# Kernel tuning notes

Measured on AMD Instinct MI355X. Metric: run time of the kernel, lower is better.

The kernel has to match this reference:

```python
import jax, jax.numpy as jnp
import numpy as np

B, C, D, Q = 256, 1000, 128, 262144
PROTO_M = 0.99   # args.proto_m
TEMP = 0.01      # hardcoded temperature in forward


def setup_inputs() -> dict:
    key = jax.random.key(0)
    ks = jax.random.split(key, 8)
    return {
        'q': jax.random.normal(ks[0], (B, D), jnp.float32),
        'k': jax.random.normal(ks[1], (B, D), jnp.float32),
        'output': jax.random.normal(ks[2], (B, C), jnp.float32),
        'output2': jax.random.normal(ks[3], (B, C), jnp.float32),
        'partial_Y': (jax.random.uniform(ks[4], (B, C)) < 0.1).astype(jnp.float32),
        'prototypes': jax.random.normal(ks[5], (C, D), jnp.float32),
        'queue': jax.random.normal(ks[6], (Q, D), jnp.float32),
        'queue_pseudo': jax.random.uniform(ks[7], (Q,), dtype=jnp.float32),
    }


def reference(q, k, output, output2, partial_Y, prototypes, queue, queue_pseudo):
    # pseudo-label selection: softmax over (detached logits * candidate mask) / T
    predicted_scores = jax.nn.softmax(jax.lax.stop_gradient(output) * partial_Y / TEMP, axis=1)
    pseudo_labels_b = jnp.argmax(predicted_scores, axis=1)  # [B] int

    # prototype scores use prototypes BEFORE the EMA update (mm snapshots values)
    logits_prot = jnp.matmul(jax.lax.stop_gradient(q), prototypes.T)  # [B, C]
    score_prot = jax.nn.softmax(logits_prot, axis=1)

    # sequential per-sample EMA scatter into prototypes (order-dependent on dup labels)
    q_detached = jax.lax.stop_gradient(q)

    def ema_step(protos, xs):
        feat, lab = xs
        new_row = protos[lab] * PROTO_M + (1.0 - PROTO_M) * feat
        return protos.at[lab].set(new_row), None

    protos, _ = jax.lax.scan(ema_step, prototypes, (q_detached, pseudo_labels_b))
    # F.normalize(p=2, dim=1) with eps=1e-12 clamp
    protos = protos / jnp.maximum(jnp.linalg.norm(protos, axis=1, keepdims=True), 1e-12)

    features = jnp.concatenate([q, k, queue], axis=0)  # [2B+Q, D]
    pseudo_labels = jnp.concatenate([
        pseudo_labels_b.astype(jnp.float32),
        pseudo_labels_b.astype(jnp.float32),
        queue_pseudo,
    ], axis=0)  # [2B+Q]

    return (output, output2, features, pseudo_labels, score_prot, protos)
```

## Files before the change

### kernel.cpp

```cpp
#include <hip/hip_runtime.h>
#include <math.h>

#define B 256
#define C 1000
#define D 128
#define QN 262144

#define OFF_FEAT   512000
#define OFF_LBL    34131968
#define OFF_SCORE  34394624
#define OFF_PROTO  34650624

#define N_Q4   (QN * D / 4)
#define N_O4   (B * C / 4)
#define N_F4   (B * D / 4)
#define N_P4   (QN / 4)

#define DST_Q4   ((OFF_FEAT + 2 * B * D) / 4)
#define DST_O24  (B * C / 4)
#define DST_QF4  (OFF_FEAT / 4)
#define DST_KF4  (OFF_FEAT / 4 + N_F4)
#define DST_P4   ((OFF_LBL + 2 * B) / 4)

#define SM_O2  (N_O4)
#define SM_Q   (2 * N_O4)
#define SM_K   (2 * N_O4 + N_F4)
#define SM_P   (2 * N_O4 + 2 * N_F4)
#define SM_TOT (2 * N_O4 + 2 * N_F4 + N_P4)

#define Q_TILES   (N_Q4 / 1024)
#define K1_TILES  640
#define POOL_BASE4 ((size_t)K1_TILES * 1024)
#define POOL_N4    ((size_t)(Q_TILES - K1_TILES) * 1024)

#define R1_SP     256
#define R1_SM     512
#define SM_BLKS   ((SM_TOT + 255) / 256)
#define R1_CP     (R1_SM + SM_BLKS)
#define K1_GRID   (R1_CP + K1_TILES)

#define K3_GRID   4096

__global__ __launch_bounds__(256) void k1_kernel(
    const float* __restrict__ q,
    const float* __restrict__ kk,
    const float* __restrict__ output,
    const float* __restrict__ output2,
    const float* __restrict__ partial_Y,
    const float* __restrict__ prototypes,
    const float4* __restrict__ queue,
    const float* __restrict__ queue_pseudo,
    int* __restrict__ labels,
    float* __restrict__ out)
{
    const int bid = blockIdx.x;
    const int tid = threadIdx.x;
    __shared__ float smem[1384];

    if (bid < B) {
        float* sv = smem;
        int*   si = (int*)(smem + 256);
        const float* row = output + (size_t)bid * C;
        const float* msk = partial_Y + (size_t)bid * C;

        float best = -INFINITY;
        int bidx = C;
        for (int c = tid; c < C; c += 256) {
            float v = row[c] * msk[c];
            if (v > best) { best = v; bidx = c; }
        }
        sv[tid] = best; si[tid] = bidx;
        __syncthreads();
        for (int s = 128; s > 0; s >>= 1) {
            if (tid < s) {
                float v2 = sv[tid + s]; int i2 = si[tid + s];
                if (v2 > sv[tid] || (v2 == sv[tid] && i2 < si[tid])) {
                    sv[tid] = v2; si[tid] = i2;
                }
            }
            __syncthreads();
        }
        if (tid == 0) {
            int lab = si[0];
            labels[bid] = lab;
            float f = (float)lab;
            out[OFF_LBL + bid]     = f;
            out[OFF_LBL + B + bid] = f;
        }
        return;
    }

    if (bid < R1_SM) {
        const int b = bid - R1_SP;
        float* logits = smem;
        float* red    = smem + C;
        float* qs     = smem + C + 256;
        if (tid < D) qs[tid] = q[(size_t)b * D + tid];
        __syncthreads();

        for (int c = tid; c < C; c += 256) {
            const float4* p4 = (const float4*)(prototypes + (size_t)c * D);
            const float4* q4 = (const float4*)qs;
            float acc = 0.f;
            #pragma unroll
            for (int d = 0; d < D / 4; ++d) {
                float4 pv = p4[d];
                float4 qv = q4[d];
                acc += pv.x * qv.x + pv.y * qv.y + pv.z * qv.z + pv.w * qv.w;
            }
            logits[c] = acc;
        }
        __syncthreads();

        float lm = -INFINITY;
        for (int c = tid; c < C; c += 256) lm = fmaxf(lm, logits[c]);
        red[tid] = lm;
        __syncthreads();
        for (int s = 128; s > 0; s >>= 1) {
            if (tid < s) red[tid] = fmaxf(red[tid], red[tid + s]);
            __syncthreads();
        }
        const float m = red[0];
        __syncthreads();

        float psum = 0.f;
        for (int c = tid; c < C; c += 256) {
            float e = expf(logits[c] - m);
            logits[c] = e;
            psum += e;
        }
        red[tid] = psum;
        __syncthreads();
        for (int s = 128; s > 0; s >>= 1) {
            if (tid < s) red[tid] += red[tid + s];
            __syncthreads();
        }
        const float denom = red[0];

        for (int c = tid; c < C; c += 256)
            out[OFF_SCORE + (size_t)b * C + c] = logits[c] / denom;
        return;
    }

    if (bid < R1_CP) {
        const size_t i = (size_t)(bid - R1_SM) * 256 + tid;
        float4* __restrict__ out4 = (float4*)out;
        if (i < SM_O2)       out4[i]                     = ((const float4*)output)[i];
        else if (i < SM_Q)   out4[DST_O24 + (i - SM_O2)] = ((const float4*)output2)[i - SM_O2];
        else if (i < SM_K)   out4[DST_QF4 + (i - SM_Q)]  = ((const float4*)q)[i - SM_Q];
        else if (i < SM_P)   out4[DST_KF4 + (i - SM_K)]  = ((const float4*)kk)[i - SM_K];
        else if (i < SM_TOT) out4[DST_P4 + (i - SM_P)]   = ((const float4*)queue_pseudo)[i - SM_P];
        return;
    }

    const size_t base = (size_t)(bid - R1_CP) * 1024 + tid;
    float4* __restrict__ dst = (float4*)out + DST_Q4;
    float4 a = queue[base];
    float4 b = queue[base + 256];
    float4 c = queue[base + 512];
    float4 d = queue[base + 768];
    dst[base]       = a;
    dst[base + 256] = b;
    dst[base + 512] = c;
    dst[base + 768] = d;
}

__global__ __launch_bounds__(256) void ema_kernel(
    const float* __restrict__ q,
    const float* __restrict__ prototypes,
    const int* __restrict__ labels,
    float* __restrict__ out)
{
    const int ebid = blockIdx.x;
    const int tid  = threadIdx.x;
    const int half = tid >> 7;
    const int d    = tid & 127;

    __shared__ int   lab[B];
    __shared__ float ss[256];
    for (int i = tid; i < B; i += 256) lab[i] = labels[i];
    __syncthreads();

    #pragma unroll
    for (int kcl = 0; kcl < 2; ++kcl) {
        const int c = 4 * ebid + 2 * kcl + half;
        float val = prototypes[(size_t)c * D + d];
        #pragma unroll 8
        for (int b = 0; b < B; ++b) {
            if (lab[b] == c) {
                val = val * 0.99f + 0.01f * q[(size_t)b * D + d];
            }
        }
        ss[tid] = val * val;
        __syncthreads();
        for (int s = 64; s > 0; s >>= 1) {
            if (d < s) ss[tid] += ss[tid + s];
            __syncthreads();
        }
        float r = fmaxf(sqrtf(ss[half * 128]), 1e-12f);
        out[OFF_PROTO + (size_t)c * D + d] = val / r;
        __syncthreads();
    }
}

__global__ __launch_bounds__(256) void copy_kernel(
    const float4* __restrict__ src, float4* __restrict__ dst)
{
    const size_t stride = (size_t)gridDim.x * blockDim.x;
    for (size_t i = (size_t)blockIdx.x * blockDim.x + threadIdx.x;
         i < POOL_N4; i += stride)
        dst[i] = src[i];
}

extern "C" void kernel_launch(void* const* d_in, const int* in_sizes, int n_in,
                              void* d_out, int out_size, void* d_ws, size_t ws_size,
                              hipStream_t stream) {
    const float* q            = (const float*)d_in[0];
    const float* k            = (const float*)d_in[1];
    const float* output       = (const float*)d_in[2];
    const float* output2      = (const float*)d_in[3];
    const float* partial_Y    = (const float*)d_in[4];
    const float* prototypes   = (const float*)d_in[5];
    const float* queue        = (const float*)d_in[6];
    const float* queue_pseudo = (const float*)d_in[7];

    float* out  = (float*)d_out;
    int* labels = (int*)d_ws;

    k1_kernel<<<K1_GRID, 256, 0, stream>>>(
        q, k, output, output2, partial_Y, prototypes,
        (const float4*)queue, queue_pseudo, labels, out);

    ema_kernel<<<C / 4, 256, 0, stream>>>(q, prototypes, labels, out);

    copy_kernel<<<K3_GRID, 256, 0, stream>>>(
        (const float4*)queue + POOL_BASE4,
        (float4*)out + DST_Q4 + POOL_BASE4);
}
```

Before: 304.3 us.

## Fuse EMA prototype update with queue copy tail and rebalance copy split

Merges the EMA/normalize kernel and the remaining queue copy into a single second kernel, so the first 250 blocks do the EMA work and then every block joins a 4-way-unrolled grid-stride copy. More of the queue copy (1664 of 8192 tiles instead of 640) moves into the first kernel. This removes one kernel launch and the serialization gap between the EMA and copy stages, letting the small EMA work overlap with bandwidth-bound copying. The cost is some extra work on the EMA blocks, and the larger first kernel may delay the labels the EMA step depends on.

```diff
diff --git a/kernel.cpp b/kernel.cpp
--- a/kernel.cpp
+++ b/kernel.cpp
@@ -29,7 +29,7 @@
 #define SM_TOT (2 * N_O4 + 2 * N_F4 + N_P4)
 
 #define Q_TILES   (N_Q4 / 1024)
-#define K1_TILES  640
+#define K1_TILES  1664
 #define POOL_BASE4 ((size_t)K1_TILES * 1024)
 #define POOL_N4    ((size_t)(Q_TILES - K1_TILES) * 1024)
 
@@ -39,7 +39,9 @@
 #define R1_CP     (R1_SM + SM_BLKS)
 #define K1_GRID   (R1_CP + K1_TILES)
 
-#define K3_GRID   4096
+#define R2_EMA    250
+#define K2_GRID   2048
+#define TOT_THR2  ((size_t)K2_GRID * 256)
 
 __global__ __launch_bounds__(256) void k1_kernel(
     const float* __restrict__ q,
@@ -165,51 +167,61 @@
     dst[base + 768] = d;
 }
 
-__global__ __launch_bounds__(256) void ema_kernel(
+__global__ __launch_bounds__(256, 8) void k2_kernel(
     const float* __restrict__ q,
     const float* __restrict__ prototypes,
+    const float4* __restrict__ queue,
     const int* __restrict__ labels,
     float* __restrict__ out)
 {
-    const int ebid = blockIdx.x;
-    const int tid  = threadIdx.x;
-    const int half = tid >> 7;
-    const int d    = tid & 127;
-
-    __shared__ int   lab[B];
-    __shared__ float ss[256];
-    for (int i = tid; i < B; i += 256) lab[i] = labels[i];
-    __syncthreads();
-
-    #pragma unroll
-    for (int kcl = 0; kcl < 2; ++kcl) {
-        const int c = 4 * ebid + 2 * kcl + half;
-        float val = prototypes[(size_t)c * D + d];
-        #pragma unroll 8
-        for (int b = 0; b < B; ++b) {
-            if (lab[b] == c) {
-                val = val * 0.99f + 0.01f * q[(size_t)b * D + d];
-            }
-        }
-        ss[tid] = val * val;
-        __syncthreads();
-        for (int s = 64; s > 0; s >>= 1) {
-            if (d < s) ss[tid] += ss[tid + s];
-            __syncthreads();
-        }
-        float r = fmaxf(sqrtf(ss[half * 128]), 1e-12f);
-        out[OFF_PROTO + (size_t)c * D + d] = val / r;
-        __syncthreads();
-    }
-}
-
-__global__ __launch_bounds__(256) void copy_kernel(
-    const float4* __restrict__ src, float4* __restrict__ dst)
-{
-    const size_t stride = (size_t)gridDim.x * blockDim.x;
-    for (size_t i = (size_t)blockIdx.x * blockDim.x + threadIdx.x;
-         i < POOL_N4; i += stride)
-        dst[i] = src[i];
+    const int bid = blockIdx.x;
+    const int tid = threadIdx.x;
+
+    if (bid < R2_EMA) {
+        __shared__ int   lab[B];
+        __shared__ float ss[256];
+        const int half = tid >> 7;
+        const int d    = tid & 127;
+        for (int i = tid; i < B; i += 256) lab[i] = labels[i];
+        __syncthreads();
+
+        #pragma unroll
+        for (int kcl = 0; kcl < 2; ++kcl) {
+            const int c = 4 * bid + 2 * kcl + half;
+            float val = prototypes[(size_t)c * D + d];
+            #pragma unroll 8
+            for (int b = 0; b < B; ++b) {
+                if (lab[b] == c) {
+                    val = val * 0.99f + 0.01f * q[(size_t)b * D + d];
+                }
+            }
+            ss[tid] = val * val;
+            __syncthreads();
+            for (int s = 64; s > 0; s >>= 1) {
+                if (d < s) ss[tid] += ss[tid + s];
+                __syncthreads();
+            }
+            float r = fmaxf(sqrtf(ss[half * 128]), 1e-12f);
+            out[OFF_PROTO + (size_t)c * D + d] = val / r;
+            __syncthreads();
+        }
+    }
+
+    const float4* __restrict__ srcq = queue + POOL_BASE4;
+    float4* __restrict__ dstq = (float4*)out + DST_Q4 + POOL_BASE4;
+    size_t i = (size_t)bid * 256 + tid;
+    for (; i + 3 * TOT_THR2 < POOL_N4; i += 4 * TOT_THR2) {
+        float4 a = srcq[i];
+        float4 b = srcq[i +     TOT_THR2];
+        float4 c = srcq[i + 2 * TOT_THR2];
+        float4 d = srcq[i + 3 * TOT_THR2];
+        dstq[i]                = a;
+        dstq[i +     TOT_THR2] = b;
+        dstq[i + 2 * TOT_THR2] = c;
+        dstq[i + 3 * TOT_THR2] = d;
+    }
+    for (; i < POOL_N4; i += TOT_THR2)
+        dstq[i] = srcq[i];
 }
 
 extern "C" void kernel_launch(void* const* d_in, const int* in_sizes, int n_in,
@@ -231,9 +243,6 @@
         q, k, output, output2, partial_Y, prototypes,
         (const float4*)queue, queue_pseudo, labels, out);
 
-    ema_kernel<<<C / 4, 256, 0, stream>>>(q, prototypes, labels, out);
-
-    copy_kernel<<<K3_GRID, 256, 0, stream>>>(
-        (const float4*)queue + POOL_BASE4,
-        (float4*)out + DST_Q4 + POOL_BASE4);
+    k2_kernel<<<K2_GRID, 256, 0, stream>>>(
+        q, prototypes, (const float4*)queue, labels, out);
 }
```

Measured after the change: 275.7 us. 1.1x faster.
